# Kernel tuning notes

Hardware: AMD Instinct MI355X
Metric: run time of the kernel (lower is better)

The kernel has to match this reference:

```python
import jax, jax.numpy as jnp
import numpy as np

SCALE = 1.0

def setup_inputs() -> dict:
    key = jax.random.key(0)
    ks = jax.random.split(key, 7)
    B, S, I, O, R = 4, 4096, 1024, 1024, 256
    return {
        "x": jax.random.normal(ks[0], (B, S, I), dtype=jnp.float32),
        "base_weight": jax.random.normal(ks[1], (3 * O, I), dtype=jnp.float32) * 0.02,
        "base_bias": jax.random.normal(ks[2], (3 * O,), dtype=jnp.float32) * 0.02,
        "vera_A": jax.random.normal(ks[3], (R, I), dtype=jnp.float32) * 0.02,
        "vera_B": jax.random.normal(ks[4], (O, R), dtype=jnp.float32) * 0.02,
        "vera_d": jax.random.normal(ks[5], (2, R), dtype=jnp.float32) * 0.1,
        "vera_b": jax.random.normal(ks[6], (2, O), dtype=jnp.float32) * 0.1,
    }

def reference(x, base_weight, base_bias, vera_A, vera_B, vera_d, vera_b):
    # delta[k] = scale * diag(vera_b[k]) @ B @ diag(vera_d[k]) @ A  for k in {K, V}
    # implemented as (b[:,None]*B) @ (d[:,None]*A), batched over k via einsum
    O, I = vera_B.shape[0], vera_A.shape[1]
    deltas = SCALE * jnp.einsum("ko,or,kr,ri->koi", vera_b, vera_B, vera_d, vera_A)
    delta = deltas.reshape(2 * O, I)  # (2*O, I) stacked K,V deltas
    # kv_only=True: Q rows get zero delta, then K,V deltas
    zeros = jnp.zeros((base_weight.shape[0] - 2 * O, I), dtype=base_weight.dtype)
    full_delta = jnp.concatenate([zeros, delta], axis=0)  # (3*O, I)
    weight = base_weight + full_delta
    # linear: x @ weight.T + bias -> (B, S, 3*O)
    return jnp.einsum("bsi,oi->bso", x, weight) + base_bias
```

## Files before the change

kernel.cpp:

```cpp
#include <hip/hip_runtime.h>
#include <hip/hip_bf16.h>
#include <cstdint>
#include <cstddef>

typedef __bf16 bf16_t;
typedef __bf16 bf16x8 __attribute__((ext_vector_type(8)));
typedef __bf16 bf16x4 __attribute__((ext_vector_type(4)));
typedef float  f32x4  __attribute__((ext_vector_type(4)));

#define M_DIM 16384
#define N_DIM 3072
#define K_DIM 1024
#define R_DIM 256
#define O_DIM 1024

#define BM 256
#define BN 256
#define BK 64
#define NTILE (N_DIM / BN)
#define GRID_GEMM ((M_DIM / BM) * NTILE)
#define CHUNK_XCD (GRID_GEMM / 8)
#define SMEM_BYTES 131072

#define REGN(c, isB, kh) ((c) * 32768 + (isB) * 16384 + (kh) * 8192)

__device__ __forceinline__ void gload_lds16(const bf16_t* g, bf16_t* l) {
  __builtin_amdgcn_global_load_lds(
      (__attribute__((address_space(1))) void*)(g),
      (__attribute__((address_space(3))) void*)(l), 16, 0, 0);
}

__global__ __launch_bounds__(256) void prep_all(
    const float* __restrict__ x,
    const float* __restrict__ base_w,
    const float* __restrict__ vA,
    const float* __restrict__ vB,
    const float* __restrict__ vd,
    const float* __restrict__ vb,
    bf16_t* __restrict__ Wf,
    bf16_t* __restrict__ xh)
{
  const int blk = blockIdx.x;
  const int t = threadIdx.x;

  if (blk >= 384) {
    const size_t base = ((size_t)(blk - 384) * 256 + t) * 8;
    const f32x4 v0 = *(const f32x4*)(x + base);
    const f32x4 v1 = *(const f32x4*)(x + base + 4);
    bf16x8 o;
    o[0] = (bf16_t)v0[0]; o[1] = (bf16_t)v0[1]; o[2] = (bf16_t)v0[2]; o[3] = (bf16_t)v0[3];
    o[4] = (bf16_t)v1[0]; o[5] = (bf16_t)v1[1]; o[6] = (bf16_t)v1[2]; o[7] = (bf16_t)v1[3];
    *(bf16x8*)(xh + base) = o;
    return;
  }

  if (blk < 128) {
    const float* src = base_w + (size_t)blk * 8 * K_DIM;
    bf16_t*      dst = Wf + (size_t)blk * 8 * K_DIM;
#pragma unroll
    for (int rr = 0; rr < 8; ++rr) {
      const f32x4 v = *(const f32x4*)(src + rr * K_DIM + t * 4);
      bf16x4 ov;
      ov[0] = (bf16_t)v[0]; ov[1] = (bf16_t)v[1];
      ov[2] = (bf16_t)v[2]; ov[3] = (bf16_t)v[3];
      *(bf16x4*)(dst + rr * K_DIM + t * 4) = ov;
    }
    return;
  }

  const int rb = (blk - 128) * 8;
  const int k  = rb >> 10;
  const int ob = rb & 1023;

  __shared__ float coeffT[R_DIM][8];
  {
    const int r = t;
    const float d = vd[k * R_DIM + r];
#pragma unroll
    for (int rr = 0; rr < 8; ++rr) {
      const int o = ob + rr;
      coeffT[r][rr] = vb[k * O_DIM + o] * vB[(size_t)o * R_DIM + r] * d;
    }
  }
  __syncthreads();

  float acc[8][4];
#pragma unroll
  for (int rr = 0; rr < 8; ++rr)
#pragma unroll
    for (int c = 0; c < 4; ++c) acc[rr][c] = 0.0f;

  for (int r = 0; r < R_DIM; ++r) {
    const f32x4 av = *(const f32x4*)(vA + (size_t)r * K_DIM + t * 4);
    const f32x4 c0 = *(const f32x4*)&coeffT[r][0];
    const f32x4 c1 = *(const f32x4*)&coeffT[r][4];
#pragma unroll
    for (int rr = 0; rr < 8; ++rr) {
      const float cc = (rr < 4) ? c0[rr] : c1[rr - 4];
      acc[rr][0] += cc * av[0];
      acc[rr][1] += cc * av[1];
      acc[rr][2] += cc * av[2];
      acc[rr][3] += cc * av[3];
    }
  }

#pragma unroll
  for (int rr = 0; rr < 8; ++rr) {
    const size_t row = (size_t)(1024 + rb + rr);
    const f32x4 bw = *(const f32x4*)(base_w + row * K_DIM + t * 4);
    bf16x4 ov;
    ov[0] = (bf16_t)(bw[0] + acc[rr][0]);
    ov[1] = (bf16_t)(bw[1] + acc[rr][1]);
    ov[2] = (bf16_t)(bw[2] + acc[rr][2]);
    ov[3] = (bf16_t)(bw[3] + acc[rr][3]);
    *(bf16x4*)(Wf + row * K_DIM + t * 4) = ov;
  }
}

__global__ __launch_bounds__(512, 2) void gemm_qkv(
    const bf16_t* __restrict__ Xh,
    const bf16_t* __restrict__ W,
    const float*  __restrict__ bias,
    float* __restrict__ out)
{
  extern __shared__ __align__(16) bf16_t sm[];

  const int rawbid = blockIdx.x;
  const int bid = (rawbid & 7) * CHUNK_XCD + (rawbid >> 3);
  const int mt = bid / NTILE, nt = bid % NTILE;
  const int m0 = mt * BM, n0 = nt * BN;

  const int t = threadIdx.x;
  const int lane = t & 63;
  const int w = t >> 6;
  const int wm = w >> 2;
  const int wn = w & 3;

  const int srow = t >> 2;
  const int sig  = (t & 3) ^ ((t >> 3) & 3);
  const bf16_t* pA0 = Xh + (size_t)(m0 + srow) * K_DIM + sig * 8;
  const bf16_t* pA1 = pA0 + (size_t)128 * K_DIM;
  const bf16_t* pB0 = W  + (size_t)(n0 + srow) * K_DIM + sig * 8;
  const bf16_t* pB1 = pB0 + (size_t)128 * K_DIM;

  const int rA = wm * 128 + (lane & 15);
  const int rB = wn * 64  + (lane & 15);
  const int aoff = rA * 32 + (((lane >> 4) ^ ((rA >> 1) & 3)) * 8);
  const int boff = rB * 32 + (((lane >> 4) ^ ((rB >> 1) & 3)) * 8);

  f32x4 acc[8][4];
#pragma unroll
  for (int i = 0; i < 8; ++i)
#pragma unroll
    for (int j = 0; j < 4; ++j) acc[i][j] = (f32x4){0.f, 0.f, 0.f, 0.f};

#define STAGE(isB, c, kh, kb)                                              \
  do {                                                                     \
    const bf16_t* g0 = ((isB) ? pB0 : pA0) + (kb) + (kh) * 32;             \
    const bf16_t* g1 = ((isB) ? pB1 : pA1) + (kb) + (kh) * 32;             \
    bf16_t* l = sm + REGN(c, isB, kh) + w * 512;                           \
    gload_lds16(g0, l);                                                    \
    gload_lds16(g1, l + 4096);                                             \
  } while (0)

#define LOADA(c, kh)                                                       \
  {                                                                        \
    const bf16_t* base_ = sm + REGN(c, 0, kh) + aoff;                      \
    _Pragma("unroll") for (int i = 0; i < 8; ++i)                          \
        a[i] = *(const bf16x8*)(base_ + i * 512);                          \
  }

#define LOADB2(c, kh, j0)                                                  \
  {                                                                        \
    const bf16_t* base_ = sm + REGN(c, 1, kh) + boff;                      \
    b[j0]     = *(const bf16x8*)(base_ + (j0) * 512);                      \
    b[j0 + 1] = *(const bf16x8*)(base_ + ((j0) + 1) * 512);                \
  }

#define MFMA2(j0)                                                          \
  __builtin_amdgcn_s_setprio(1);                                           \
  _Pragma("unroll") for (int i = 0; i < 8; ++i) {                          \
    acc[i][j0] = __builtin_amdgcn_mfma_f32_16x16x32_bf16(                  \
        a[i], b[j0], acc[i][j0], 0, 0, 0);                                 \
    acc[i][(j0) + 1] = __builtin_amdgcn_mfma_f32_16x16x32_bf16(            \
        a[i], b[(j0) + 1], acc[i][(j0) + 1], 0, 0, 0);                     \
  }                                                                        \
  __builtin_amdgcn_s_setprio(0);

#define WAITV(n) asm volatile("s_waitcnt vmcnt(" #n ")" ::: "memory")
#define BARRIER()                                                          \
  __builtin_amdgcn_s_barrier();                                            \
  asm volatile("" ::: "memory")

  bf16x8 a[8], b[4];

  STAGE(0, 0, 0, 0);
  STAGE(1, 0, 0, 0);
  STAGE(0, 0, 1, 0);
  STAGE(1, 0, 1, 0);
  WAITV(4);
  BARRIER();

  for (int tt = 0; tt < 15; ++tt) {
    const int c = tt & 1, cn = c ^ 1;
    const int kb = (tt + 1) * BK;

    LOADA(c, 0);
    LOADB2(c, 0, 0);
    STAGE(0, cn, 0, kb);
    BARRIER();
    MFMA2(0);
    BARRIER();

    LOADB2(c, 0, 2);
    STAGE(1, cn, 0, kb);
    WAITV(4);
    BARRIER();
    MFMA2(2);
    BARRIER();

    LOADA(c, 1);
    LOADB2(c, 1, 0);
    STAGE(0, cn, 1, kb);
    BARRIER();
    MFMA2(0);
    BARRIER();

    LOADB2(c, 1, 2);
    STAGE(1, cn, 1, kb);
    WAITV(4);
    BARRIER();
    MFMA2(2);
    BARRIER();
  }

  LOADA(1, 0);
  LOADB2(1, 0, 0);
  BARRIER();
  MFMA2(0);
  BARRIER();

  LOADB2(1, 0, 2);
  WAITV(0);
  BARRIER();
  MFMA2(2);
  BARRIER();

  LOADA(1, 1);
  LOADB2(1, 1, 0);
  BARRIER();
  MFMA2(0);
  BARRIER();

  LOADB2(1, 1, 2);
  BARRIER();
  MFMA2(2);

  const int colg = lane & 15;
  const int rq = (lane >> 4) * 4;
#pragma unroll
  for (int j = 0; j < 4; ++j) {
    const int n = n0 + wn * 64 + j * 16 + colg;
    const float bv = bias[n];
#pragma unroll
    for (int i = 0; i < 8; ++i) {
      const size_t mb = (size_t)(m0 + wm * 128 + i * 16 + rq);
#pragma unroll
      for (int r = 0; r < 4; ++r)
        out[(mb + r) * N_DIM + n] = acc[i][j][r] + bv;
    }
  }
#undef STAGE
#undef LOADA
#undef LOADB2
#undef MFMA2
#undef WAITV
#undef BARRIER
}

#define FBM 128
#define FBN 128
#define FBK 32
template <bool PRECONV>
__global__ __launch_bounds__(256) void gemm128(
    const bf16_t* __restrict__ Xh,
    const float*  __restrict__ Xf,
    const bf16_t* __restrict__ W,
    const float*  __restrict__ bias,
    float* __restrict__ out)
{
  __shared__ bf16_t As[FBM * FBK];
  __shared__ bf16_t Bs[FBN * FBK];

  const int rawbid = blockIdx.x;
  const int nblk = (M_DIM / FBM) * (N_DIM / FBN);
  const int bid = (rawbid & 7) * (nblk / 8) + (rawbid >> 3);
  const int nt = bid % (N_DIM / FBN);
  const int mt = bid / (N_DIM / FBN);
  const int m0 = mt * FBM;
  const int n0 = nt * FBN;

  const int t = threadIdx.x;
  const int lane = t & 63;
  const int w = t >> 6;
  const int wm = w >> 1;
  const int wn = w & 1;

  const int r0 = t >> 2;
  const int c0 = (t & 3) * 8;

  const bf16_t* gB0 = W + (size_t)(n0 + r0) * K_DIM + c0;
  const bf16_t* gB1 = gB0 + (size_t)64 * K_DIM;
  bf16_t* lA0 = As + r0 * FBK + c0;
  bf16_t* lA1 = As + (r0 + 64) * FBK + c0;
  bf16_t* lB0 = Bs + r0 * FBK + c0;
  bf16_t* lB1 = Bs + (r0 + 64) * FBK + c0;

  const bf16_t* gA0h = nullptr; const bf16_t* gA1h = nullptr;
  const float*  gA0f = nullptr; const float*  gA1f = nullptr;
  if constexpr (PRECONV) {
    gA0h = Xh + (size_t)(m0 + r0) * K_DIM + c0;
    gA1h = gA0h + (size_t)64 * K_DIM;
  } else {
    gA0f = Xf + (size_t)(m0 + r0) * K_DIM + c0;
    gA1f = gA0f + (size_t)64 * K_DIM;
  }

  f32x4 acc[4][4];
#pragma unroll
  for (int i = 0; i < 4; ++i)
#pragma unroll
    for (int j = 0; j < 4; ++j) acc[i][j] = (f32x4){0.f, 0.f, 0.f, 0.f};

  const int row_a = wm * 64 + (lane & 15);
  const int row_b = wn * 64 + (lane & 15);
  const int kb = (lane >> 4) * 8;

  for (int k0 = 0; k0 < K_DIM; k0 += FBK) {
    if constexpr (PRECONV) {
      gload_lds16(gA0h + k0, lA0);
      gload_lds16(gA1h + k0, lA1);
    } else {
      const f32x4 u0 = *(const f32x4*)(gA0f + k0);
      const f32x4 u1 = *(const f32x4*)(gA0f + k0 + 4);
      const f32x4 u2 = *(const f32x4*)(gA1f + k0);
      const f32x4 u3 = *(const f32x4*)(gA1f + k0 + 4);
      bf16x8 a0, a1;
#pragma unroll
      for (int c = 0; c < 4; ++c) {
        a0[c] = (bf16_t)u0[c]; a0[c + 4] = (bf16_t)u1[c];
        a1[c] = (bf16_t)u2[c]; a1[c + 4] = (bf16_t)u3[c];
      }
      *(bf16x8*)lA0 = a0;
      *(bf16x8*)lA1 = a1;
    }
    gload_lds16(gB0 + k0, lB0);
    gload_lds16(gB1 + k0, lB1);
    __syncthreads();

    bf16x8 a[4], b[4];
#pragma unroll
    for (int i = 0; i < 4; ++i)
      a[i] = *(const bf16x8*)(As + (row_a + i * 16) * FBK + kb);
#pragma unroll
    for (int j = 0; j < 4; ++j)
      b[j] = *(const bf16x8*)(Bs + (row_b + j * 16) * FBK + kb);

#pragma unroll
    for (int i = 0; i < 4; ++i)
#pragma unroll
      for (int j = 0; j < 4; ++j)
        acc[i][j] = __builtin_amdgcn_mfma_f32_16x16x32_bf16(a[i], b[j], acc[i][j], 0, 0, 0);

    __syncthreads();
  }

  const int colg = lane & 15;
  const int rq = (lane >> 4) * 4;
#pragma unroll
  for (int j = 0; j < 4; ++j) {
    const int n = n0 + wn * 64 + j * 16 + colg;
    const float bv = bias[n];
#pragma unroll
    for (int i = 0; i < 4; ++i) {
      const size_t mb = (size_t)(m0 + wm * 64 + i * 16 + rq);
#pragma unroll
      for (int r = 0; r < 4; ++r)
        out[(mb + r) * N_DIM + n] = acc[i][j][r] + bv;
    }
  }
}

extern "C" void kernel_launch(void* const* d_in, const int* in_sizes, int n_in,
                              void* d_out, int out_size, void* d_ws, size_t ws_size,
                              hipStream_t stream) {
  const float* x      = (const float*)d_in[0];
  const float* base_w = (const float*)d_in[1];
  const float* base_b = (const float*)d_in[2];
  const float* vA     = (const float*)d_in[3];
  const float* vB     = (const float*)d_in[4];
  const float* vd     = (const float*)d_in[5];
  const float* vb     = (const float*)d_in[6];
  float* out = (float*)d_out;

  const size_t xh_off   = 8u * 1024 * 1024;
  const size_t xh_bytes = (size_t)M_DIM * K_DIM * sizeof(bf16_t);

  bf16_t* Wf = (bf16_t*)d_ws;
  const bool preconv = ws_size >= xh_off + xh_bytes;
  bf16_t* Xh = preconv ? (bf16_t*)((char*)d_ws + xh_off) : nullptr;

  static int smem_ok = -1;
  if (smem_ok < 0) {
    hipError_t e = hipFuncSetAttribute(
        reinterpret_cast<const void*>(&gemm_qkv),
        hipFuncAttributeMaxDynamicSharedMemorySize, SMEM_BYTES);
    smem_ok = (e == hipSuccess) ? 1 : 0;
  }

  prep_all<<<preconv ? 8576 : 384, 256, 0, stream>>>(x, base_w, vA, vB, vd, vb, Wf, Xh);

  if (preconv && smem_ok == 1) {
    gemm_qkv<<<GRID_GEMM, 512, SMEM_BYTES, stream>>>(Xh, Wf, base_b, out);
  } else if (preconv) {
    gemm128<true><<<(M_DIM / FBM) * (N_DIM / FBN), 256, 0, stream>>>(
        Xh, nullptr, Wf, base_b, out);
  } else {
    gemm128<false><<<(M_DIM / FBM) * (N_DIM / FBN), 256, 0, stream>>>(
        nullptr, x, Wf, base_b, out);
  }
}
```

Measured before the change: 413.1 us.

## Switch main GEMM to 32x32x16 bf16 MFMA with matching LDS fragment loads

Replaces the 16x16x32 MFMA tiling in the 256x256 GEMM with 32x32x16 MFMAs, reorganizing per-wave accumulators into 4x2 f32x16 blocks. The LDS fragment addressing and swizzle are changed to match the 32-row layout, and the epilogue is rewritten for the 32x32 output layout. Larger MFMA tiles reuse each fragment more, which cuts the LDS reads per FLOP and the instruction count. The cost is different register pressure and a less coalesced output store pattern.

```diff
diff --git a/kernel.cpp b/kernel.cpp
--- a/kernel.cpp
+++ b/kernel.cpp
@@ -7,6 +7,7 @@
 typedef __bf16 bf16x8 __attribute__((ext_vector_type(8)));
 typedef __bf16 bf16x4 __attribute__((ext_vector_type(4)));
 typedef float  f32x4  __attribute__((ext_vector_type(4)));
+typedef float  f32x16 __attribute__((ext_vector_type(16)));
 
 #define M_DIM 16384
 #define N_DIM 3072
@@ -143,16 +144,19 @@
   const bf16_t* pB0 = W  + (size_t)(n0 + srow) * K_DIM + sig * 8;
   const bf16_t* pB1 = pB0 + (size_t)128 * K_DIM;
 
-  const int rA = wm * 128 + (lane & 15);
-  const int rB = wn * 64  + (lane & 15);
-  const int aoff = rA * 32 + (((lane >> 4) ^ ((rA >> 1) & 3)) * 8);
-  const int boff = rB * 32 + (((lane >> 4) ^ ((rB >> 1) & 3)) * 8);
-
-  f32x4 acc[8][4];
-#pragma unroll
-  for (int i = 0; i < 8; ++i)
-#pragma unroll
-    for (int j = 0; j < 4; ++j) acc[i][j] = (f32x4){0.f, 0.f, 0.f, 0.f};
+  const int l31 = lane & 31;
+  const int hi  = lane >> 5;
+  const int swz = (l31 >> 1) & 3;
+  const int sA  = (wm * 128 + l31) * 32;
+  const int sB  = (wn * 64  + l31) * 32;
+  const int sl0 = ((0 + hi) ^ swz) * 8;
+  const int sl1 = ((2 + hi) ^ swz) * 8;
+
+  f32x16 acc[4][2];
+#pragma unroll
+  for (int i = 0; i < 4; ++i)
+#pragma unroll
+    for (int j = 0; j < 2; ++j) acc[i][j] = (f32x16)0.0f;
 
 #define STAGE(isB, c, kh, kb)                                              \
   do {                                                                     \
@@ -165,26 +169,26 @@
 
 #define LOADA(c, kh)                                                       \
   {                                                                        \
-    const bf16_t* base_ = sm + REGN(c, 0, kh) + aoff;                      \
-    _Pragma("unroll") for (int i = 0; i < 8; ++i)                          \
-        a[i] = *(const bf16x8*)(base_ + i * 512);                          \
-  }
-
-#define LOADB2(c, kh, j0)                                                  \
+    const bf16_t* base_ = sm + REGN(c, 0, kh) + sA;                        \
+    _Pragma("unroll") for (int i = 0; i < 4; ++i) {                        \
+      a[i][0] = *(const bf16x8*)(base_ + i * 1024 + sl0);                  \
+      a[i][1] = *(const bf16x8*)(base_ + i * 1024 + sl1);                  \
+    }                                                                      \
+  }
+
+#define LOADB(c, kh, j)                                                    \
   {                                                                        \
-    const bf16_t* base_ = sm + REGN(c, 1, kh) + boff;                      \
-    b[j0]     = *(const bf16x8*)(base_ + (j0) * 512);                      \
-    b[j0 + 1] = *(const bf16x8*)(base_ + ((j0) + 1) * 512);                \
-  }
-
-#define MFMA2(j0)                                                          \
+    const bf16_t* base_ = sm + REGN(c, 1, kh) + sB + (j) * 1024;           \
+    b[j][0] = *(const bf16x8*)(base_ + sl0);                               \
+    b[j][1] = *(const bf16x8*)(base_ + sl1);                               \
+  }
+
+#define MFMA8(j)                                                           \
   __builtin_amdgcn_s_setprio(1);                                           \
-  _Pragma("unroll") for (int i = 0; i < 8; ++i) {                          \
-    acc[i][j0] = __builtin_amdgcn_mfma_f32_16x16x32_bf16(                  \
-        a[i], b[j0], acc[i][j0], 0, 0, 0);                                 \
-    acc[i][(j0) + 1] = __builtin_amdgcn_mfma_f32_16x16x32_bf16(            \
-        a[i], b[(j0) + 1], acc[i][(j0) + 1], 0, 0, 0);                     \
-  }                                                                        \
+  _Pragma("unroll") for (int ks = 0; ks < 2; ++ks)                         \
+    _Pragma("unroll") for (int i = 0; i < 4; ++i)                          \
+      acc[i][j] = __builtin_amdgcn_mfma_f32_32x32x16_bf16(                 \
+          a[i][ks], b[j][ks], acc[i][j], 0, 0, 0);                         \
   __builtin_amdgcn_s_setprio(0);
 
 #define WAITV(n) asm volatile("s_waitcnt vmcnt(" #n ")" ::: "memory")
@@ -192,7 +196,7 @@
   __builtin_amdgcn_s_barrier();                                            \
   asm volatile("" ::: "memory")
 
-  bf16x8 a[8], b[4];
+  bf16x8 a[4][2], b[2][2];
 
   STAGE(0, 0, 0, 0);
   STAGE(1, 0, 0, 0);
@@ -206,74 +210,75 @@
     const int kb = (tt + 1) * BK;
 
     LOADA(c, 0);
-    LOADB2(c, 0, 0);
+    LOADB(c, 0, 0);
     STAGE(0, cn, 0, kb);
     BARRIER();
-    MFMA2(0);
-    BARRIER();
-
-    LOADB2(c, 0, 2);
+    MFMA8(0);
+    BARRIER();
+
+    LOADB(c, 0, 1);
     STAGE(1, cn, 0, kb);
     WAITV(4);
     BARRIER();
-    MFMA2(2);
+    MFMA8(1);
     BARRIER();
 
     LOADA(c, 1);
-    LOADB2(c, 1, 0);
+    LOADB(c, 1, 0);
     STAGE(0, cn, 1, kb);
     BARRIER();
-    MFMA2(0);
-    BARRIER();
-
-    LOADB2(c, 1, 2);
+    MFMA8(0);
+    BARRIER();
+
+    LOADB(c, 1, 1);
     STAGE(1, cn, 1, kb);
     WAITV(4);
     BARRIER();
-    MFMA2(2);
+    MFMA8(1);
     BARRIER();
   }
 
   LOADA(1, 0);
-  LOADB2(1, 0, 0);
-  BARRIER();
-  MFMA2(0);
-  BARRIER();
-
-  LOADB2(1, 0, 2);
+  LOADB(1, 0, 0);
+  BARRIER();
+  MFMA8(0);
+  BARRIER();
+
+  LOADB(1, 0, 1);
   WAITV(0);
   BARRIER();
-  MFMA2(2);
+  MFMA8(1);
   BARRIER();
 
   LOADA(1, 1);
-  LOADB2(1, 1, 0);
-  BARRIER();
-  MFMA2(0);
-  BARRIER();
-
-  LOADB2(1, 1, 2);
-  BARRIER();
-  MFMA2(2);
-
-  const int colg = lane & 15;
-  const int rq = (lane >> 4) * 4;
-#pragma unroll
-  for (int j = 0; j < 4; ++j) {
-    const int n = n0 + wn * 64 + j * 16 + colg;
+  LOADB(1, 1, 0);
+  BARRIER();
+  MFMA8(0);
+  BARRIER();
+
+  LOADB(1, 1, 1);
+  BARRIER();
+  MFMA8(1);
+
+  const int hi4 = hi * 4;
+#pragma unroll
+  for (int j = 0; j < 2; ++j) {
+    const int n = n0 + wn * 64 + j * 32 + l31;
     const float bv = bias[n];
 #pragma unroll
-    for (int i = 0; i < 8; ++i) {
-      const size_t mb = (size_t)(m0 + wm * 128 + i * 16 + rq);
-#pragma unroll
-      for (int r = 0; r < 4; ++r)
-        out[(mb + r) * N_DIM + n] = acc[i][j][r] + bv;
+    for (int i = 0; i < 4; ++i) {
+      const size_t mb = (size_t)(m0 + wm * 128 + i * 32 + hi4);
+#pragma unroll
+      for (int r = 0; r < 16; ++r) {
+        const size_t row = mb + (r & 3) + 8 * (r >> 2);
+        out[row * N_DIM + n] = acc[i][j][r] + bv;
+      }
     }
   }
 #undef STAGE
 #undef LOADA
-#undef LOADB2
-#undef MFMA2
+#undef LOADB
+#undef MFMA8
 #undef WAITV
 #undef BARRIER
 }
```

New measurement: 395.8 us. 4.2% less time.
